# Optimization experiments

Hardware: AMD Instinct MI355X
Metric: run time of the kernel (lower is better)

## Reference

```python
import jax, jax.numpy as jnp
import numpy as np

# B groups, N packed tokens/group, D model dim, H heads, L layers, FF mlp hidden,
# M samples packed per group, C classes, PD patch_dim, NF/NT freq/time pos tables
B, N, D, H, L, FF, M, C, PD, NF, NT = 4, 1024, 768, 12, 12, 3072, 8, 527, 256, 8, 64


def _ln(x, g, b, eps=1e-6):
    m = jnp.mean(x, -1, keepdims=True)
    v = jnp.mean((x - m) ** 2, -1, keepdims=True)
    return (x - m) * jax.lax.rsqrt(v + eps) * g + b


def _attn(xq, xkv, Wq, bq, Wkv, bkv, Wo, bo, allowed):
    # allowed: [b, i, j] bool; faithful to source: NO 1/sqrt(d_head) scaling.
    b, i, _ = xq.shape
    j = xkv.shape[1]
    q = (xq @ Wq + bq).reshape(b, i, H, -1).transpose(0, 2, 1, 3)
    k, v = jnp.split(xkv @ Wkv + bkv, 2, axis=-1)
    k = k.reshape(b, j, H, -1).transpose(0, 2, 1, 3)
    v = v.reshape(b, j, H, -1).transpose(0, 2, 1, 3)
    dots = jnp.einsum('bhid,bhjd->bhij', q, k)
    neg = -jnp.finfo(dots.dtype).max
    dots = jnp.where(allowed[:, None, :, :], dots, neg)
    a = jax.nn.softmax(dots, axis=-1)
    out = jnp.einsum('bhij,bhjd->bhid', a, v).transpose(0, 2, 1, 3).reshape(b, i, -1)
    return out @ Wo + bo


def setup_inputs() -> dict:
    ks = iter(jax.random.split(jax.random.key(0), 48))
    rn = lambda shape, s=0.02: jax.random.normal(next(ks), shape, jnp.float32) * s
    return {
        'patches': jax.random.normal(next(ks), (B, N, PD), jnp.float32),
        'sample_ids': jnp.sort(jax.random.randint(next(ks), (B, N), 0, M), axis=-1).astype(jnp.int32),
        'key_pad': jnp.ones((B, N), bool),
        'freq_idx': jax.random.randint(next(ks), (B, N), 0, NF).astype(jnp.int32),
        'time_idx': jax.random.randint(next(ks), (B, N), 0, NT).astype(jnp.int32),
        'patch_W': rn((PD, D)), 'patch_b': jnp.zeros((D,)),
        'pos_f': rn((NF, D), 1.0), 'pos_t': rn((NT, D), 1.0),
        'ln1_g': jnp.ones((L, D)), 'ln1_b': jnp.zeros((L, D)),
        'Wq': rn((L, D, D)), 'bq': jnp.zeros((L, D)),
        'Wkv': rn((L, D, 2 * D)), 'bkv': jnp.zeros((L, 2 * D)),
        'Wo': rn((L, D, D)), 'bo': jnp.zeros((L, D)),
        'ln2_g': jnp.ones((L, D)), 'ln2_b': jnp.zeros((L, D)),
        'W1': rn((L, D, FF)), 'b1': jnp.zeros((L, FF)),
        'W2': rn((L, FF, D)), 'b2': jnp.zeros((L, D)),
        'norm_g': jnp.ones((D,)), 'norm_b': jnp.zeros((D,)),
        'pool_q': rn((D,), 1.0),
        'pool_Wq': rn((D, D)), 'pool_bq': jnp.zeros((D,)),
        'pool_Wkv': rn((D, 2 * D)), 'pool_bkv': jnp.zeros((2 * D,)),
        'pool_Wo': rn((D, D)), 'pool_bo': jnp.zeros((D,)),
        'mln_g': jnp.ones((D,)), 'mln_b': jnp.zeros((D,)),
        'head_W': rn((D, C)), 'head_b': jnp.zeros((C,)),
    }


def reference(patches, sample_ids, key_pad, freq_idx, time_idx, patch_W, patch_b, pos_f, pos_t,
              ln1_g, ln1_b, Wq, bq, Wkv, bkv, Wo, bo, ln2_g, ln2_b, W1, b1, W2, b2,
              norm_g, norm_b, pool_q, pool_Wq, pool_bq, pool_Wkv, pool_bkv, pool_Wo, pool_bo,
              mln_g, mln_b, head_W, head_b):
    # patch embed + factorized freq/time positional embedding
    x = patches @ patch_W + patch_b + pos_f[freq_idx] + pos_t[time_idx]  # [B, N, D]
    # block-diagonal attention within each packed sample + key-padding mask
    same = sample_ids[:, :, None] == sample_ids[:, None, :]
    allowed = same & key_pad[:, None, :]
    for l in range(L):
        h = _ln(x, ln1_g[l], ln1_b[l])
        x = x + _attn(h, h, Wq[l], bq[l], Wkv[l], bkv[l], Wo[l], bo[l], allowed)
        h = _ln(x, ln2_g[l], ln2_b[l])
        x = x + (jax.nn.gelu(h @ W1[l] + b1[l], approximate=False) @ W2[l] + b2[l])
    x = _ln(x, norm_g, norm_b)
    # attention pooling: one learned query per packed sample, attends only its own tokens
    queries = jnp.broadcast_to(pool_q, (B, M, D))
    pool_allowed = (sample_ids[:, None, :] == jnp.arange(M)[None, :, None]) & key_pad[:, None, :]
    pooled = _attn(queries, x, pool_Wq, pool_bq, pool_Wkv, pool_bkv, pool_Wo, pool_bo, pool_allowed)
    return _ln(pooled, mln_g, mln_b) @ head_W + head_b  # [B, M, C]
```

## Files before the change

kernel.cpp:

```cpp
#include <hip/hip_runtime.h>
#include <hip/hip_bf16.h>
#include <math.h>

#define BB   4
#define NN   1024
#define DD   768
#define HHH  12
#define LLL  12
#define FFD  3072
#define MMM  8
#define CCC  527
#define PDIM 256

typedef unsigned short u16;
typedef __attribute__((ext_vector_type(8))) short bf16x8;
typedef __attribute__((ext_vector_type(4))) float f32x4;

__device__ inline float b2f(u16 x) {
    union { float f; unsigned u; } c; c.u = ((unsigned)x) << 16; return c.f;
}
__device__ inline u16 f2b(float f) {
    __hip_bfloat16 h = __float2bfloat16(f);
    return *reinterpret_cast<u16*>(&h);
}

__device__ __forceinline__ float gelu_fast(float v) {
    const float x = v * 0.70710678118f;
    const float xa = fabsf(x);
    const float tt = 1.f / (1.f + 0.3275911f * xa);
    const float poly = tt * (0.254829592f + tt * (-0.284496736f + tt * (1.421413741f +
                       tt * (-1.453152027f + tt * 1.061405429f))));
    float er = 1.f - poly * __expf(-xa * xa);
    er = (x < 0.f) ? -er : er;
    return 0.5f * v * (1.f + er);
}

__device__ __forceinline__ void gl_lds16(const u16* g, const u16* l) {
    __builtin_amdgcn_global_load_lds(
        (const __attribute__((address_space(1))) unsigned int*)(unsigned long long)g,
        (__attribute__((address_space(3))) unsigned int*)(unsigned)(unsigned long long)l,
        16, 0, 0);
}

__global__ void k_pad_norm(const void* __restrict__ p, unsigned char* __restrict__ out, int n) {
    __shared__ int isInt;
    const int t = threadIdx.x;
    if (t == 0) isInt = 1;
    __syncthreads();
    const unsigned* up = (const unsigned*)p;
    for (int i = t; i < n / 4; i += 1024) {
        unsigned v = up[i];
        if (v > 1u) isInt = 0;
    }
    __syncthreads();
    const int* ip = (const int*)p;
    const unsigned char* cp = (const unsigned char*)p;
    const int mode = isInt;
    for (int i = t; i < n; i += 1024)
        out[i] = mode ? (unsigned char)(ip[i] != 0) : (unsigned char)(cp[i] != 0);
}

__global__ __launch_bounds__(256) void k_transpose_cvt(
    const float* __restrict__ src, u16* __restrict__ dst,
    int K, int N, long srcLS, long dstLS)
{
    __shared__ float t[64][33];
    const float* s = src + (size_t)blockIdx.z * srcLS;
    u16* d = dst + (size_t)blockIdx.z * dstLS;
    const int n0 = blockIdx.x * 32, k0 = blockIdx.y * 64;
    const int tx = threadIdx.x & 31, ty = threadIdx.x >> 5;
    #pragma unroll
    for (int i = 0; i < 8; i++)
        t[ty * 8 + i][tx] = s[(size_t)(k0 + ty * 8 + i) * N + n0 + tx];
    __syncthreads();
    #pragma unroll
    for (int p = 0; p < 4; p++) {
        const int ny = p * 8 + ty;
        union { u16 h[2]; unsigned u; } o;
        o.h[0] = f2b(t[2 * tx][ny]);
        o.h[1] = f2b(t[2 * tx + 1][ny]);
        *(unsigned*)&d[(size_t)(n0 + ny) * K + k0 + 2 * tx] = o.u;
    }
}

__global__ __launch_bounds__(256) void k_cvt(const float* __restrict__ s, u16* __restrict__ d, int n4) {
    int i = blockIdx.x * 256 + threadIdx.x;
    if (i >= n4) return;
    float4 v = ((const float4*)s)[i];
    union { u16 h[4]; uint2 u; } o;
    o.h[0] = f2b(v.x); o.h[1] = f2b(v.y); o.h[2] = f2b(v.z); o.h[3] = f2b(v.w);
    ((uint2*)d)[i] = o.u;
}

__global__ __launch_bounds__(256) void k_bias_pack(const float* __restrict__ bq,
                                                   const float* __restrict__ bkv,
                                                   float* __restrict__ bqkv) {
    int i = blockIdx.x * 256 + threadIdx.x;
    if (i >= LLL * 2304) return;
    int l = i / 2304, c = i % 2304;
    bqkv[i] = (c < 768) ? bq[l * 768 + c] : bkv[l * 1536 + (c - 768)];
}

__global__ void k_ranges(const int* __restrict__ sid, int2* __restrict__ qr, int2* __restrict__ pr) {
    int b = blockIdx.x, t = threadIdx.x;
    const int* s = sid + b * NN;
    if (t < 16) {
        int lo_id = s[t * 64], hi_id = s[t * 64 + 63];
        int lo = 0, hi = NN;
        while (lo < hi) { int mid = (lo + hi) >> 1; if (s[mid] < lo_id) lo = mid + 1; else hi = mid; }
        int l2 = 0, h2 = NN;
        while (l2 < h2) { int mid = (l2 + h2) >> 1; if (s[mid] <= hi_id) l2 = mid + 1; else h2 = mid; }
        qr[b * 16 + t] = make_int2(lo, l2);
    }
    if (t < MMM) {
        int l2 = 0, h2 = NN;
        while (l2 < h2) { int mid = (l2 + h2) >> 1; if (s[mid] < t) l2 = mid + 1; else h2 = mid; }
        int l3 = 0, h3 = NN;
        while (l3 < h3) { int mid = (l3 + h3) >> 1; if (s[mid] <= t) l3 = mid + 1; else h3 = mid; }
        pr[b * MMM + t] = make_int2(l2, l3);
    }
}

__device__ inline void stv(u16* p, float v) { *p = f2b(v); }
__device__ inline void stv(float* p, float v) { *p = v; }

template <typename OT>
__global__ __launch_bounds__(256) void k_ln(const float* __restrict__ x,
                                            const float* __restrict__ g,
                                            const float* __restrict__ b,
                                            OT* __restrict__ out) {
    int row = blockIdx.x;
    const float* xr = x + (size_t)row * DD;
    int t = threadIdx.x;
    float v[3], s1 = 0.f, s2 = 0.f;
    #pragma unroll
    for (int i = 0; i < 3; i++) { v[i] = xr[t + i * 256]; s1 += v[i]; s2 += v[i] * v[i]; }
    #pragma unroll
    for (int o = 32; o; o >>= 1) { s1 += __shfl_xor(s1, o); s2 += __shfl_xor(s2, o); }
    __shared__ float a1[4], a2[4];
    int w = t >> 6;
    if ((t & 63) == 0) { a1[w] = s1; a2[w] = s2; }
    __syncthreads();
    s1 = a1[0] + a1[1] + a1[2] + a1[3];
    s2 = a2[0] + a2[1] + a2[2] + a2[3];
    float mean = s1 * (1.f / DD);
    float var = s2 * (1.f / DD) - mean * mean;
    float rstd = rsqrtf(fmaxf(var, 0.f) + 1e-6f);
    #pragma unroll
    for (int i = 0; i < 3; i++) {
        int c = t + i * 256;
        stv(&out[(size_t)row * DD + c], (v[i] - mean) * rstd * g[c] + b[c]);
    }
}

template <int EPI, int BM>
__global__ __launch_bounds__(256) void k_gemm(
    const u16* __restrict__ A, int lda,
    const u16* __restrict__ Bt, int ldb,
    const float* __restrict__ bias,
    float* __restrict__ Cf, u16* __restrict__ Cb,
    const float* __restrict__ resid,
    int ldc, int K,
    const int* __restrict__ fidx = nullptr, const int* __restrict__ tidx = nullptr,
    const float* __restrict__ pf = nullptr, const float* __restrict__ pt = nullptr)
{
    constexpr int NR  = (BM == 128) ? 4 : 2;
    constexpr int ASZ = BM * 32;
    constexpr int BSZ = 128 * 32;
    __shared__ __align__(16) u16 As[3][ASZ];
    __shared__ __align__(16) u16 Bs[3][BSZ];
    const int gx = gridDim.x;
    const int nwg = gx * gridDim.y;
    int bid = blockIdx.y * gx + blockIdx.x;
    if ((nwg & 7) == 0) bid = (bid & 7) * (nwg >> 3) + (bid >> 3);
    const int row0 = (bid / gx) * BM, col0 = (bid % gx) * 128;
    const int t = threadIdx.x;
    const int w = t >> 6, lane = t & 63;
    const int wr = (BM == 128) ? (w >> 1) * 64 : 0;
    const int wc = (BM == 128) ? (w & 1) * 64 : w * 32;
    const int fr = lane & 15, fg = lane >> 4;
    const int srow = t >> 2, sseg = (t & 3) * 8;
    const u16* Ap = A + (size_t)(row0 + srow) * lda + sseg;
    const u16* Bp = Bt + (size_t)(col0 + srow) * ldb + sseg;
    const size_t lstep = (size_t)64 * lda, bstep = (size_t)64 * ldb;

    auto stage = [&](int buf, int k0) {
        #pragma unroll
        for (int i = 0; i < BM / 64; i++)
            gl_lds16(Ap + i * lstep + k0, &As[buf][i * 2048 + t * 8]);
        #pragma unroll
        for (int i = 0; i < 2; i++)
            gl_lds16(Bp + i * bstep + k0, &Bs[buf][i * 2048 + t * 8]);
    };

    f32x4 acc[4][NR];
    #pragma unroll
    for (int m = 0; m < 4; m++)
        #pragma unroll
        for (int n = 0; n < NR; n++) acc[m][n] = (f32x4){0.f, 0.f, 0.f, 0.f};

    const int nt = K >> 5;
    stage(0, 0);
    stage(1, 32);

    for (int kt = 0; kt < nt; ++kt) {
        if (kt + 1 < nt) {
            if constexpr (BM == 128) asm volatile("s_waitcnt vmcnt(4)" ::: "memory");
            else                     asm volatile("s_waitcnt vmcnt(3)" ::: "memory");
        } else {
            asm volatile("s_waitcnt vmcnt(0)" ::: "memory");
        }
        __builtin_amdgcn_s_barrier();
        __builtin_amdgcn_sched_barrier(0);
        if (kt + 2 < nt) stage((kt + 2) % 3, (kt + 2) * 32);
        const int cur = kt % 3;
        bf16x8 af[4], bfr[NR];
        #pragma unroll
        for (int m = 0; m < 4; m++) af[m] = *(const bf16x8*)&As[cur][(wr + m * 16 + fr) * 32 + fg * 8];
        #pragma unroll
        for (int n = 0; n < NR; n++) bfr[n] = *(const bf16x8*)&Bs[cur][(wc + n * 16 + fr) * 32 + fg * 8];
        __builtin_amdgcn_s_setprio(1);
        #pragma unroll
        for (int m = 0; m < 4; m++)
            #pragma unroll
            for (int n = 0; n < NR; n++)
                acc[m][n] = __builtin_amdgcn_mfma_f32_16x16x32_bf16(af[m], bfr[n], acc[m][n], 0, 0, 0);
        __builtin_amdgcn_s_setprio(0);
    }
    #pragma unroll
    for (int m = 0; m < 4; m++) {
        #pragma unroll
        for (int n = 0; n < NR; n++) {
            const int col = col0 + wc + n * 16 + fr;
            const float bb = bias[col];
            #pragma unroll
            for (int r = 0; r < 4; r++) {
                const size_t row = row0 + wr + m * 16 + fg * 4 + r;
                float v = acc[m][n][r] + bb;
                if (EPI == 0) {
                    Cb[row * ldc + col] = f2b(v);
                } else if (EPI == 1) {
                    Cf[row * ldc + col] = v + resid[row * ldc + col];
                } else if (EPI == 2) {
                    Cb[row * ldc + col] = f2b(gelu_fast(v));
                } else if (EPI == 3) {
                    Cf[row * ldc + col] = v;
                } else if (EPI == 5) {
                    const int fi = fidx[row], ti = tidx[row];
                    Cf[row * ldc + col] = v + pf[(size_t)fi * DD + col] + pt[(size_t)ti * DD + col];
                }
            }
        }
    }
}

__global__ __launch_bounds__(256) void k_attn(
    const u16* __restrict__ qkv,
    const int* __restrict__ sid, const unsigned char* __restrict__ pad,
    const int2* __restrict__ qr,
    u16* __restrict__ outb)
{
    __shared__ __align__(16) u16 Qs[64][72];
    __shared__ __align__(16) u16 Ks[64][72];
    __shared__ __align__(16) u16 VtL[64 * 72 + 32];
    __shared__ __align__(16) u16 Ps[4][16][72];
    __shared__ int sidq[64];
    __shared__ int sidj[64];
    __shared__ int padj[64];
    const int b = blockIdx.z, h = blockIdx.y, qt = blockIdx.x;
    const int i0 = qt * 64;
    const int t = threadIdx.x, w = t >> 6, lane = t & 63;
    const int fr = lane & 15, fg = lane >> 4;
    const int srow = t >> 2, sseg = (t & 3) * 16;
    const size_t tokbase = (size_t)b * NN;
    const u16* qbase = qkv + (tokbase + i0) * 2304 + h * 64;
    *(uint4*)&Qs[srow][sseg]     = *(const uint4*)(qbase + (size_t)srow * 2304 + sseg);
    *(uint4*)&Qs[srow][sseg + 8] = *(const uint4*)(qbase + (size_t)srow * 2304 + sseg + 8);
    if (t < 64) sidq[t] = sid[tokbase + i0 + t];
    __syncthreads();
    bf16x8 qf0 = *(const bf16x8*)&Qs[w * 16 + fr][fg * 8];
    bf16x8 qf1 = *(const bf16x8*)&Qs[w * 16 + fr][32 + fg * 8];
    const int myrow = w * 16 + fg * 4;
    float m_run[4], l_run[4];
    f32x4 oacc[4];
    #pragma unroll
    for (int r = 0; r < 4; r++) { m_run[r] = -1e30f; l_run[r] = 0.f; }
    #pragma unroll
    for (int n = 0; n < 4; n++) oacc[n] = (f32x4){0.f, 0.f, 0.f, 0.f};
    const int2 rg = qr[b * 16 + qt];
    const u16* kbase = qkv + tokbase * 2304 + 768 + h * 64;
    const u16* vbase = qkv + tokbase * 2304 + 1536 + h * 64;

    uint4 rk0, rk1, rv0, rv1;
    int rsid = 0, rpad = 0;
    const int jstart = rg.x & ~63;
    {
        const size_t ro = (size_t)(jstart + srow) * 2304;
        rk0 = *(const uint4*)(kbase + ro + sseg);
        rk1 = *(const uint4*)(kbase + ro + sseg + 8);
        rv0 = *(const uint4*)(vbase + ro + sseg);
        rv1 = *(const uint4*)(vbase + ro + sseg + 8);
        if (t < 64) { rsid = sid[tokbase + jstart + t]; rpad = pad[tokbase + jstart + t]; }
    }

    for (int j0 = jstart; j0 < rg.y; j0 += 64) {
        __syncthreads();
        *(uint4*)&Ks[srow][sseg]     = rk0;
        *(uint4*)&Ks[srow][sseg + 8] = rk1;
        {
            u16 tmp[16];
            *(uint4*)&tmp[0] = rv0;
            *(uint4*)&tmp[8] = rv1;
            const int goff = (sseg >> 4) << 3;
            #pragma unroll
            for (int e = 0; e < 16; e++)
                VtL[(sseg + e) * 72 + goff + srow] = tmp[e];
        }
        if (t < 64) { sidj[t] = rsid; padj[t] = rpad; }
        __syncthreads();
        if (j0 + 64 < rg.y) {
            const size_t ro = (size_t)(j0 + 64 + srow) * 2304;
            rk0 = *(const uint4*)(kbase + ro + sseg);
            rk1 = *(const uint4*)(kbase + ro + sseg + 8);
            rv0 = *(const uint4*)(vbase + ro + sseg);
            rv1 = *(const uint4*)(vbase + ro + sseg + 8);
            if (t < 64) { rsid = sid[tokbase + j0 + 64 + t]; rpad = pad[tokbase + j0 + 64 + t]; }
        }
        f32x4 s[4];
        __builtin_amdgcn_s_setprio(1);
        #pragma unroll
        for (int nj = 0; nj < 4; nj++) {
            bf16x8 kf0 = *(const bf16x8*)&Ks[nj * 16 + fr][fg * 8];
            bf16x8 kf1 = *(const bf16x8*)&Ks[nj * 16 + fr][32 + fg * 8];
            f32x4 a = (f32x4){0.f, 0.f, 0.f, 0.f};
            a = __builtin_amdgcn_mfma_f32_16x16x32_bf16(qf0, kf0, a, 0, 0, 0);
            a = __builtin_amdgcn_mfma_f32_16x16x32_bf16(qf1, kf1, a, 0, 0, 0);
            s[nj] = a;
        }
        __builtin_amdgcn_s_setprio(0);
        #pragma unroll
        for (int nj = 0; nj < 4; nj++) {
            const int jj = nj * 16 + fr;
            const int sj = sidj[jj];
            const int pd = padj[jj];
            #pragma unroll
            for (int r = 0; r < 4; r++) {
                const bool ok = pd && (sj == sidq[myrow + r]);
                s[nj][r] = ok ? s[nj][r] : -3e38f;
            }
        }
        float mnew[4], scale[4];
        #pragma unroll
        for (int r = 0; r < 4; r++) {
            float mx = fmaxf(fmaxf(s[0][r], s[1][r]), fmaxf(s[2][r], s[3][r]));
            #pragma unroll
            for (int o = 1; o < 16; o <<= 1) mx = fmaxf(mx, __shfl_xor(mx, o));
            mnew[r] = fmaxf(m_run[r], mx);
            scale[r] = __expf(m_run[r] - mnew[r]);
            m_run[r] = mnew[r];
        }
        #pragma unroll
        for (int r = 0; r < 4; r++) {
            float rs = 0.f;
            #pragma unroll
            for (int nj = 0; nj < 4; nj++) {
                float pv = __expf(s[nj][r] - mnew[r]);
                rs += pv;
                Ps[w][fg * 4 + r][nj * 16 + fr] = f2b(pv);
            }
            #pragma unroll
            for (int o = 1; o < 16; o <<= 1) rs += __shfl_xor(rs, o);
            l_run[r] = l_run[r] * scale[r] + rs;
        }
        #pragma unroll
        for (int n = 0; n < 4; n++)
            #pragma unroll
            for (int r = 0; r < 4; r++) oacc[n][r] *= scale[r];
        bf16x8 pa0 = *(const bf16x8*)&Ps[w][fr][fg * 8];
        bf16x8 pa1 = *(const bf16x8*)&Ps[w][fr][32 + fg * 8];
        __builtin_amdgcn_s_setprio(1);
        #pragma unroll
        for (int nd = 0; nd < 4; nd++) {
            bf16x8 vf0 = *(const bf16x8*)&VtL[(nd * 16 + fr) * 72 + nd * 8 + fg * 8];
            bf16x8 vf1 = *(const bf16x8*)&VtL[(nd * 16 + fr) * 72 + nd * 8 + 32 + fg * 8];
            oacc[nd] = __builtin_amdgcn_mfma_f32_16x16x32_bf16(pa0, vf0, oacc[nd], 0, 0, 0);
            oacc[nd] = __builtin_amdgcn_mfma_f32_16x16x32_bf16(pa1, vf1, oacc[nd], 0, 0, 0);
        }
        __builtin_amdgcn_s_setprio(0);
    }
    float inv[4];
    #pragma unroll
    for (int r = 0; r < 4; r++) inv[r] = 1.f / l_run[r];
    #pragma unroll
    for (int nd = 0; nd < 4; nd++)
        #pragma unroll
        for (int r = 0; r < 4; r++)
            outb[(tokbase + i0 + myrow + r) * DD + h * 64 + nd * 16 + fr] = f2b(oacc[nd][r] * inv[r]);
}

__global__ __launch_bounds__(64) void k_qvec(const float* __restrict__ pq, const float* __restrict__ Wq,
                                             const float* __restrict__ bq, float* __restrict__ qv) {
    int c = blockIdx.x;
    int l = threadIdx.x;
    float s = 0.f;
    #pragma unroll
    for (int d = l; d < DD; d += 64) s += pq[d] * Wq[(size_t)d * DD + c];
    #pragma unroll
    for (int o = 32; o; o >>= 1) s += __shfl_xor(s, o);
    if (l == 0) qv[c] = s + bq[c];
}

__global__ __launch_bounds__(256) void k_pool_attn(
    const float* __restrict__ qv, const u16* __restrict__ kv,
    const unsigned char* __restrict__ pad, const int2* __restrict__ pr,
    float* __restrict__ outp)
{
    const int idx = blockIdx.x;
    const int h = idx % HHH, bm = idx / HHH;
    const int b = bm >> 3, m = bm & 7;
    const int2 rg = pr[b * MMM + m];
    const int lo = rg.x, cnt = rg.y - rg.x;
    __shared__ float sc[NN];
    __shared__ float qsh[64];
    __shared__ float rbuf[4];
    __shared__ float vacc[4][64];
    if (threadIdx.x < 64) qsh[threadIdx.x] = qv[h * 64 + threadIdx.x];
    __syncthreads();
    for (int j = threadIdx.x; j < cnt; j += 256) {
        const u16* krow = kv + (size_t)(b * NN + lo + j) * 1536 + h * 64;
        float s = 0.f;
        #pragma unroll
        for (int dv = 0; dv < 8; dv++) {
            bf16x8 k8 = *(const bf16x8*)(krow + dv * 8);
            #pragma unroll
            for (int e = 0; e < 8; e++) s += qsh[dv * 8 + e] * b2f((u16)k8[e]);
        }
        sc[j] = pad[b * NN + lo + j] ? s : -3e38f;
    }
    __syncthreads();
    float mx = -3e38f;
    for (int j = threadIdx.x; j < cnt; j += 256) mx = fmaxf(mx, sc[j]);
    #pragma unroll
    for (int o = 32; o; o >>= 1) mx = fmaxf(mx, __shfl_xor(mx, o));
    if ((threadIdx.x & 63) == 0) rbuf[threadIdx.x >> 6] = mx;
    __syncthreads();
    mx = fmaxf(fmaxf(rbuf[0], rbuf[1]), fmaxf(rbuf[2], rbuf[3]));
    __syncthreads();
    float sm = 0.f;
    for (int j = threadIdx.x; j < cnt; j += 256) { float p = __expf(sc[j] - mx); sc[j] = p; sm += p; }
    #pragma unroll
    for (int o = 32; o; o >>= 1) sm += __shfl_xor(sm, o);
    if ((threadIdx.x & 63) == 0) rbuf[threadIdx.x >> 6] = sm;
    __syncthreads();
    sm = rbuf[0] + rbuf[1] + rbuf[2] + rbuf[3];
    const float inv = 1.f / sm;
    {
        const int d = threadIdx.x & 63, g = threadIdx.x >> 6;
        float acc = 0.f;
        for (int j = g; j < cnt; j += 4)
            acc += sc[j] * b2f(kv[(size_t)(b * NN + lo + j) * 1536 + 768 + h * 64 + d]);
        vacc[g][d] = acc;
        __syncthreads();
        if (g == 0)
            outp[(size_t)(b * MMM + m) * DD + h * 64 + d] =
                (vacc[0][d] + vacc[1][d] + vacc[2][d] + vacc[3][d]) * inv;
    }
}

__global__ __launch_bounds__(256) void k_small_mm(const float* __restrict__ A, const float* __restrict__ W,
                                                  const float* __restrict__ bias, float* __restrict__ out,
                                                  int N, int Kd) {
    const int row = blockIdx.y;
    const int cl = threadIdx.x & 63, kg = threadIdx.x >> 6;
    const int c = blockIdx.x * 64 + cl;
    const int cload = (c < N) ? c : (N - 1);
    __shared__ float As[DD];
    __shared__ float red[4][64];
    for (int d = threadIdx.x; d < Kd; d += 256) As[d] = A[(size_t)row * Kd + d];
    __syncthreads();
    const int kper = Kd >> 2;
    const int kbase = kg * kper;
    float s = 0.f;
    const float* w = W + (size_t)kbase * N + cload;
    #pragma unroll 4
    for (int i = 0; i < kper; i++) s += As[kbase + i] * w[(size_t)i * N];
    red[kg][cl] = s;
    __syncthreads();
    if (kg == 0 && c < N)
        out[(size_t)row * N + c] = red[0][cl] + red[1][cl] + red[2][cl] + red[3][cl] + bias[c];
}

extern "C" void kernel_launch(void* const* d_in, const int* in_sizes, int n_in,
                              void* d_out, int out_size, void* d_ws, size_t ws_size,
                              hipStream_t stream) {
    const float* patches   = (const float*)d_in[0];
    const int*   sample_ids= (const int*)d_in[1];
    const void*  key_pad_raw = (const void*)d_in[2];
    const int*   freq_idx  = (const int*)d_in[3];
    const int*   time_idx  = (const int*)d_in[4];
    const float* patch_W   = (const float*)d_in[5];
    const float* patch_b   = (const float*)d_in[6];
    const float* pos_f     = (const float*)d_in[7];
    const float* pos_t     = (const float*)d_in[8];
    const float* ln1_g     = (const float*)d_in[9];
    const float* ln1_b     = (const float*)d_in[10];
    const float* Wq        = (const float*)d_in[11];
    const float* bq        = (const float*)d_in[12];
    const float* Wkv       = (const float*)d_in[13];
    const float* bkv       = (const float*)d_in[14];
    const float* Wo        = (const float*)d_in[15];
    const float* bo        = (const float*)d_in[16];
    const float* ln2_g     = (const float*)d_in[17];
    const float* ln2_b     = (const float*)d_in[18];
    const float* W1        = (const float*)d_in[19];
    const float* b1        = (const float*)d_in[20];
    const float* W2        = (const float*)d_in[21];
    const float* b2        = (const float*)d_in[22];
    const float* norm_g    = (const float*)d_in[23];
    const float* norm_b    = (const float*)d_in[24];
    const float* pool_q    = (const float*)d_in[25];
    const float* pool_Wq   = (const float*)d_in[26];
    const float* pool_bq   = (const float*)d_in[27];
    const float* pool_Wkv  = (const float*)d_in[28];
    const float* pool_bkv  = (const float*)d_in[29];
    const float* pool_Wo   = (const float*)d_in[30];
    const float* pool_bo   = (const float*)d_in[31];
    const float* mln_g     = (const float*)d_in[32];
    const float* mln_b     = (const float*)d_in[33];
    const float* head_W    = (const float*)d_in[34];
    const float* head_b    = (const float*)d_in[35];
    float* outp = (float*)d_out;
    (void)in_sizes; (void)n_in; (void)out_size; (void)ws_size;

    char* ws = (char*)d_ws;
    size_t off = 0;
    auto alloc = [&](size_t bytes) -> void* {
        void* p = (void*)(ws + off);
        off += (bytes + 255) & ~(size_t)255;
        return p;
    };
    u16* WqkvT    = (u16*)alloc((size_t)LLL * 2304 * 768 * 2);
    u16* WoT      = (u16*)alloc((size_t)LLL * 768 * 768 * 2);
    u16* W1T      = (u16*)alloc((size_t)LLL * 3072 * 768 * 2);
    u16* W2T      = (u16*)alloc((size_t)LLL * 768 * 3072 * 2);
    u16* patchWT  = (u16*)alloc((size_t)768 * 256 * 2);
    u16* poolWkvT = (u16*)alloc((size_t)1536 * 768 * 2);
    float* bqkv   = (float*)alloc((size_t)LLL * 2304 * 4);
    unsigned char* pad_u8 = (unsigned char*)alloc(BB * NN);
    float* x      = (float*)alloc((size_t)4096 * 768 * 4);
    u16* hbuf     = (u16*)alloc((size_t)4096 * 768 * 2);
    u16* qkvb     = (u16*)alloc((size_t)4096 * 2304 * 2);
    u16* attno    = (u16*)alloc((size_t)4096 * 768 * 2);
    u16* mid      = (u16*)alloc((size_t)4096 * 3072 * 2);
    u16* patch_bf = mid;
    u16* xn       = attno;
    u16* poolkv   = qkvb;
    float* qvec   = (float*)alloc(768 * 4);
    float* pooled_pre = (float*)alloc(32 * 768 * 4);
    float* pooled2    = (float*)alloc(32 * 768 * 4);
    float* mlnout     = (float*)alloc(32 * 768 * 4);
    int2* qr = (int2*)alloc(4 * 16 * sizeof(int2));
    int2* pr = (int2*)alloc(4 * 8 * sizeof(int2));

    k_pad_norm<<<1, 1024, 0, stream>>>(key_pad_raw, pad_u8, BB * NN);
    k_transpose_cvt<<<dim3(24, 12, LLL), 256, 0, stream>>>(Wq, WqkvT, 768, 768, (long)768 * 768, (long)2304 * 768);
    k_transpose_cvt<<<dim3(48, 12, LLL), 256, 0, stream>>>(Wkv, WqkvT + (size_t)768 * 768, 768, 1536, (long)768 * 1536, (long)2304 * 768);
    k_transpose_cvt<<<dim3(24, 12, LLL), 256, 0, stream>>>(Wo, WoT, 768, 768, (long)768 * 768, (long)768 * 768);
    k_transpose_cvt<<<dim3(96, 12, LLL), 256, 0, stream>>>(W1, W1T, 768, 3072, (long)768 * 3072, (long)3072 * 768);
    k_transpose_cvt<<<dim3(24, 48, LLL), 256, 0, stream>>>(W2, W2T, 3072, 768, (long)3072 * 768, (long)768 * 3072);
    k_transpose_cvt<<<dim3(24, 4, 1), 256, 0, stream>>>(patch_W, patchWT, 256, 768, 0, 0);
    k_transpose_cvt<<<dim3(48, 12, 1), 256, 0, stream>>>(pool_Wkv, poolWkvT, 768, 1536, 0, 0);
    k_cvt<<<1024, 256, 0, stream>>>(patches, patch_bf, 4096 * 256 / 4);
    k_bias_pack<<<(LLL * 2304 + 255) / 256, 256, 0, stream>>>(bq, bkv, bqkv);
    k_ranges<<<4, 64, 0, stream>>>(sample_ids, qr, pr);

    k_gemm<5, 64><<<dim3(6, 64), 256, 0, stream>>>(patch_bf, 256, patchWT, 256, patch_b, x, nullptr, nullptr,
                                                   768, 256, freq_idx, time_idx, pos_f, pos_t);

    for (int l = 0; l < LLL; l++) {
        k_ln<u16><<<4096, 256, 0, stream>>>(x, ln1_g + l * 768, ln1_b + l * 768, hbuf);
        k_gemm<0, 128><<<dim3(18, 32), 256, 0, stream>>>(hbuf, 768, WqkvT + (size_t)l * 2304 * 768, 768,
                                                         bqkv + l * 2304, nullptr, qkvb, nullptr, 2304, 768);
        k_attn<<<dim3(16, 12, 4), 256, 0, stream>>>(qkvb, sample_ids, pad_u8, qr, attno);
        k_gemm<1, 64><<<dim3(6, 64), 256, 0, stream>>>(attno, 768, WoT + (size_t)l * 768 * 768, 768,
                                                       bo + l * 768, x, nullptr, x, 768, 768);
        k_ln<u16><<<4096, 256, 0, stream>>>(x, ln2_g + l * 768, ln2_b + l * 768, hbuf);
        k_gemm<2, 128><<<dim3(24, 32), 256, 0, stream>>>(hbuf, 768, W1T + (size_t)l * 3072 * 768, 768,
                                                         b1 + l * 3072, nullptr, mid, nullptr, 3072, 768);
        k_gemm<1, 64><<<dim3(6, 64), 256, 0, stream>>>(mid, 3072, W2T + (size_t)l * 768 * 3072, 3072,
                                                       b2 + l * 768, x, nullptr, x, 768, 3072);
    }

    k_ln<u16><<<4096, 256, 0, stream>>>(x, norm_g, norm_b, xn);
    k_gemm<0, 128><<<dim3(12, 32), 256, 0, stream>>>(xn, 768, poolWkvT, 768, pool_bkv, nullptr, poolkv, nullptr, 1536, 768);
    k_qvec<<<768, 64, 0, stream>>>(pool_q, pool_Wq, pool_bq, qvec);
    k_pool_attn<<<BB * MMM * HHH, 256, 0, stream>>>(qvec, poolkv, pad_u8, pr, pooled_pre);
    k_small_mm<<<dim3(12, 32), 256, 0, stream>>>(pooled_pre, pool_Wo, pool_bo, pooled2, 768, 768);
    k_ln<float><<<32, 256, 0, stream>>>(pooled2, mln_g, mln_b, mlnout);
    k_small_mm<<<dim3(9, 32), 256, 0, stream>>>(mlnout, head_W, head_b, outp, 527, 768);
}
```

Baseline: 2.063 ms.

## Double-buffer K/V tiles in attention and use one wave per row in layernorm

The attention kernel now keeps two shared-memory K/V buffers. The next tile is written while the current one is being computed, which cuts the two barriers per iteration down to one. Q staging and P share a single pooled LDS buffer. Layernorm now gives each row to one 64-lane wave with float4 loads and vector stores, which removes the cross-wave shared reduction and barrier. The trade-off is more LDS use per attention block, which could lower occupancy.

```diff
diff --git a/kernel.cpp b/kernel.cpp
--- a/kernel.cpp
+++ b/kernel.cpp
@@ -121,35 +121,44 @@
     }
 }
 
-__device__ inline void stv(u16* p, float v) { *p = f2b(v); }
-__device__ inline void stv(float* p, float v) { *p = v; }
-
 template <typename OT>
 __global__ __launch_bounds__(256) void k_ln(const float* __restrict__ x,
                                             const float* __restrict__ g,
                                             const float* __restrict__ b,
                                             OT* __restrict__ out) {
-    int row = blockIdx.x;
+    const int row = blockIdx.x * 4 + (threadIdx.x >> 6);
+    const int l = threadIdx.x & 63;
     const float* xr = x + (size_t)row * DD;
-    int t = threadIdx.x;
-    float v[3], s1 = 0.f, s2 = 0.f;
-    #pragma unroll
-    for (int i = 0; i < 3; i++) { v[i] = xr[t + i * 256]; s1 += v[i]; s2 += v[i] * v[i]; }
+    float4 v[3];
+    float s1 = 0.f, s2 = 0.f;
+    #pragma unroll
+    for (int k = 0; k < 3; k++) {
+        v[k] = *(const float4*)(xr + k * 256 + l * 4);
+        s1 += v[k].x + v[k].y + v[k].z + v[k].w;
+        s2 += v[k].x * v[k].x + v[k].y * v[k].y + v[k].z * v[k].z + v[k].w * v[k].w;
+    }
     #pragma unroll
     for (int o = 32; o; o >>= 1) { s1 += __shfl_xor(s1, o); s2 += __shfl_xor(s2, o); }
-    __shared__ float a1[4], a2[4];
-    int w = t >> 6;
-    if ((t & 63) == 0) { a1[w] = s1; a2[w] = s2; }
-    __syncthreads();
-    s1 = a1[0] + a1[1] + a1[2] + a1[3];
-    s2 = a2[0] + a2[1] + a2[2] + a2[3];
-    float mean = s1 * (1.f / DD);
-    float var = s2 * (1.f / DD) - mean * mean;
-    float rstd = rsqrtf(fmaxf(var, 0.f) + 1e-6f);
-    #pragma unroll
-    for (int i = 0; i < 3; i++) {
-        int c = t + i * 256;
-        stv(&out[(size_t)row * DD + c], (v[i] - mean) * rstd * g[c] + b[c]);
+    const float mean = s1 * (1.f / DD);
+    const float var = s2 * (1.f / DD) - mean * mean;
+    const float rstd = rsqrtf(fmaxf(var, 0.f) + 1e-6f);
+    #pragma unroll
+    for (int k = 0; k < 3; k++) {
+        const int c = k * 256 + l * 4;
+        const float4 gg = *(const float4*)(g + c);
+        const float4 bb = *(const float4*)(b + c);
+        const float r0 = (v[k].x - mean) * rstd * gg.x + bb.x;
+        const float r1 = (v[k].y - mean) * rstd * gg.y + bb.y;
+        const float r2 = (v[k].z - mean) * rstd * gg.z + bb.z;
+        const float r3 = (v[k].w - mean) * rstd * gg.w + bb.w;
+        if constexpr (sizeof(OT) == 2) {
+            union { u16 h[4]; uint2 u; } o;
+            o.h[0] = f2b(r0); o.h[1] = f2b(r1); o.h[2] = f2b(r2); o.h[3] = f2b(r3);
+            *(uint2*)&out[(size_t)row * DD + c] = o.u;
+        } else {
+            float4 o = make_float4(r0, r1, r2, r3);
+            *(float4*)&out[(size_t)row * DD + c] = o;
+        }
     }
 }
 
@@ -260,26 +269,29 @@
     const int2* __restrict__ qr,
     u16* __restrict__ outb)
 {
-    __shared__ __align__(16) u16 Qs[64][72];
-    __shared__ __align__(16) u16 Ks[64][72];
-    __shared__ __align__(16) u16 VtL[64 * 72 + 32];
-    __shared__ __align__(16) u16 Ps[4][16][72];
+    __shared__ __align__(16) u16 pool[2 * 4608 + 2 * 4640 + 4608];
+    u16* const K0  = pool;
+    u16* const K1  = pool + 4608;
+    u16* const V0  = pool + 9216;
+    u16* const V1  = pool + 9216 + 4640;
+    u16* const PsB = pool + 9216 + 9280;
     __shared__ int sidq[64];
-    __shared__ int sidj[64];
-    __shared__ int padj[64];
+    __shared__ int sidj[2][64];
+    __shared__ int padj[2][64];
     const int b = blockIdx.z, h = blockIdx.y, qt = blockIdx.x;
     const int i0 = qt * 64;
     const int t = threadIdx.x, w = t >> 6, lane = t & 63;
     const int fr = lane & 15, fg = lane >> 4;
     const int srow = t >> 2, sseg = (t & 3) * 16;
+    const int goff = (sseg >> 4) << 3;
     const size_t tokbase = (size_t)b * NN;
     const u16* qbase = qkv + (tokbase + i0) * 2304 + h * 64;
-    *(uint4*)&Qs[srow][sseg]     = *(const uint4*)(qbase + (size_t)srow * 2304 + sseg);
-    *(uint4*)&Qs[srow][sseg + 8] = *(const uint4*)(qbase + (size_t)srow * 2304 + sseg + 8);
+    *(uint4*)&K1[srow * 72 + sseg]     = *(const uint4*)(qbase + (size_t)srow * 2304 + sseg);
+    *(uint4*)&K1[srow * 72 + sseg + 8] = *(const uint4*)(qbase + (size_t)srow * 2304 + sseg + 8);
     if (t < 64) sidq[t] = sid[tokbase + i0 + t];
     __syncthreads();
-    bf16x8 qf0 = *(const bf16x8*)&Qs[w * 16 + fr][fg * 8];
-    bf16x8 qf1 = *(const bf16x8*)&Qs[w * 16 + fr][32 + fg * 8];
+    const bf16x8 qf0 = *(const bf16x8*)&K1[(w * 16 + fr) * 72 + fg * 8];
+    const bf16x8 qf1 = *(const bf16x8*)&K1[(w * 16 + fr) * 72 + 32 + fg * 8];
     const int myrow = w * 16 + fg * 4;
     float m_run[4], l_run[4];
     f32x4 oacc[4];
@@ -290,48 +302,50 @@
     const int2 rg = qr[b * 16 + qt];
     const u16* kbase = qkv + tokbase * 2304 + 768 + h * 64;
     const u16* vbase = qkv + tokbase * 2304 + 1536 + h * 64;
+    const int jstart = rg.x & ~63;
+    const int ntiles = (rg.y - jstart + 63) >> 6;
 
     uint4 rk0, rk1, rv0, rv1;
     int rsid = 0, rpad = 0;
-    const int jstart = rg.x & ~63;
-    {
-        const size_t ro = (size_t)(jstart + srow) * 2304;
+    auto load_tile = [&](int tile) {
+        const size_t ro = (size_t)(jstart + tile * 64 + srow) * 2304;
         rk0 = *(const uint4*)(kbase + ro + sseg);
         rk1 = *(const uint4*)(kbase + ro + sseg + 8);
         rv0 = *(const uint4*)(vbase + ro + sseg);
         rv1 = *(const uint4*)(vbase + ro + sseg + 8);
-        if (t < 64) { rsid = sid[tokbase + jstart + t]; rpad = pad[tokbase + jstart + t]; }
-    }
-
-    for (int j0 = jstart; j0 < rg.y; j0 += 64) {
-        __syncthreads();
-        *(uint4*)&Ks[srow][sseg]     = rk0;
-        *(uint4*)&Ks[srow][sseg + 8] = rk1;
-        {
-            u16 tmp[16];
-            *(uint4*)&tmp[0] = rv0;
-            *(uint4*)&tmp[8] = rv1;
-            const int goff = (sseg >> 4) << 3;
-            #pragma unroll
-            for (int e = 0; e < 16; e++)
-                VtL[(sseg + e) * 72 + goff + srow] = tmp[e];
-        }
-        if (t < 64) { sidj[t] = rsid; padj[t] = rpad; }
-        __syncthreads();
-        if (j0 + 64 < rg.y) {
-            const size_t ro = (size_t)(j0 + 64 + srow) * 2304;
-            rk0 = *(const uint4*)(kbase + ro + sseg);
-            rk1 = *(const uint4*)(kbase + ro + sseg + 8);
-            rv0 = *(const uint4*)(vbase + ro + sseg);
-            rv1 = *(const uint4*)(vbase + ro + sseg + 8);
-            if (t < 64) { rsid = sid[tokbase + j0 + 64 + t]; rpad = pad[tokbase + j0 + 64 + t]; }
+        if (t < 64) { rsid = sid[tokbase + jstart + tile * 64 + t]; rpad = pad[tokbase + jstart + tile * 64 + t]; }
+    };
+    auto write_tile = [&](u16* kb, u16* vb, int slot) {
+        *(uint4*)&kb[srow * 72 + sseg]     = rk0;
+        *(uint4*)&kb[srow * 72 + sseg + 8] = rk1;
+        u16 tmp[16];
+        *(uint4*)&tmp[0] = rv0;
+        *(uint4*)&tmp[8] = rv1;
+        #pragma unroll
+        for (int e = 0; e < 16; e++)
+            vb[(sseg + e) * 72 + goff + srow] = tmp[e];
+        if (t < 64) { sidj[slot][t] = rsid; padj[slot][t] = rpad; }
+    };
+
+    load_tile(0);
+    write_tile(K0, V0, 0);
+    if (ntiles > 1) load_tile(1);
+    __syncthreads();
+
+    for (int tt = 0; tt < ntiles; ++tt) {
+        const int cb = tt & 1;
+        u16* const kb = cb ? K1 : K0;
+        u16* const vb = cb ? V1 : V0;
+        if (tt + 1 < ntiles) {
+            write_tile(cb ? K0 : K1, cb ? V0 : V1, cb ^ 1);
+            if (tt + 2 < ntiles) load_tile(tt + 2);
         }
         f32x4 s[4];
         __builtin_amdgcn_s_setprio(1);
         #pragma unroll
         for (int nj = 0; nj < 4; nj++) {
-            bf16x8 kf0 = *(const bf16x8*)&Ks[nj * 16 + fr][fg * 8];
-            bf16x8 kf1 = *(const bf16x8*)&Ks[nj * 16 + fr][32 + fg * 8];
+            bf16x8 kf0 = *(const bf16x8*)&kb[(nj * 16 + fr) * 72 + fg * 8];
+            bf16x8 kf1 = *(const bf16x8*)&kb[(nj * 16 + fr) * 72 + 32 + fg * 8];
             f32x4 a = (f32x4){0.f, 0.f, 0.f, 0.f};
             a = __builtin_amdgcn_mfma_f32_16x16x32_bf16(qf0, kf0, a, 0, 0, 0);
             a = __builtin_amdgcn_mfma_f32_16x16x32_bf16(qf1, kf1, a, 0, 0, 0);
@@ -341,8 +355,8 @@
         #pragma unroll
         for (int nj = 0; nj < 4; nj++) {
             const int jj = nj * 16 + fr;
-            const int sj = sidj[jj];
-            const int pd = padj[jj];
+            const int sj = sidj[cb][jj];
+            const int pd = padj[cb][jj];
             #pragma unroll
             for (int r = 0; r < 4; r++) {
                 const bool ok = pd && (sj == sidq[myrow + r]);
@@ -366,7 +380,7 @@
             for (int nj = 0; nj < 4; nj++) {
                 float pv = __expf(s[nj][r] - mnew[r]);
                 rs += pv;
-                Ps[w][fg * 4 + r][nj * 16 + fr] = f2b(pv);
+                PsB[(w * 16 + fg * 4 + r) * 72 + nj * 16 + fr] = f2b(pv);
             }
             #pragma unroll
             for (int o = 1; o < 16; o <<= 1) rs += __shfl_xor(rs, o);
@@ -376,17 +390,18 @@
         for (int n = 0; n < 4; n++)
             #pragma unroll
             for (int r = 0; r < 4; r++) oacc[n][r] *= scale[r];
-        bf16x8 pa0 = *(const bf16x8*)&Ps[w][fr][fg * 8];
-        bf16x8 pa1 = *(const bf16x8*)&Ps[w][fr][32 + fg * 8];
+        bf16x8 pa0 = *(const bf16x8*)&PsB[(w * 16 + fr) * 72 + fg * 8];
+        bf16x8 pa1 = *(const bf16x8*)&PsB[(w * 16 + fr) * 72 + 32 + fg * 8];
         __builtin_amdgcn_s_setprio(1);
         #pragma unroll
         for (int nd = 0; nd < 4; nd++) {
-            bf16x8 vf0 = *(const bf16x8*)&VtL[(nd * 16 + fr) * 72 + nd * 8 + fg * 8];
-            bf16x8 vf1 = *(const bf16x8*)&VtL[(nd * 16 + fr) * 72 + nd * 8 + 32 + fg * 8];
+            bf16x8 vf0 = *(const bf16x8*)&vb[(nd * 16 + fr) * 72 + nd * 8 + fg * 8];
+            bf16x8 vf1 = *(const bf16x8*)&vb[(nd * 16 + fr) * 72 + nd * 8 + 32 + fg * 8];
             oacc[nd] = __builtin_amdgcn_mfma_f32_16x16x32_bf16(pa0, vf0, oacc[nd], 0, 0, 0);
             oacc[nd] = __builtin_amdgcn_mfma_f32_16x16x32_bf16(pa1, vf1, oacc[nd], 0, 0, 0);
         }
         __builtin_amdgcn_s_setprio(0);
+        __syncthreads();
     }
     float inv[4];
     #pragma unroll
@@ -578,24 +593,24 @@
                                                    768, 256, freq_idx, time_idx, pos_f, pos_t);
 
     for (int l = 0; l < LLL; l++) {
-        k_ln<u16><<<4096, 256, 0, stream>>>(x, ln1_g + l * 768, ln1_b + l * 768, hbuf);
+        k_ln<u16><<<1024, 256, 0, stream>>>(x, ln1_g + l * 768, ln1_b + l * 768, hbuf);
         k_gemm<0, 128><<<dim3(18, 32), 256, 0, stream>>>(hbuf, 768, WqkvT + (size_t)l * 2304 * 768, 768,
                                                          bqkv + l * 2304, nullptr, qkvb, nullptr, 2304, 768);
         k_attn<<<dim3(16, 12, 4), 256, 0, stream>>>(qkvb, sample_ids, pad_u8, qr, attno);
         k_gemm<1, 64><<<dim3(6, 64), 256, 0, stream>>>(attno, 768, WoT + (size_t)l * 768 * 768, 768,
                                                        bo + l * 768, x, nullptr, x, 768, 768);
-        k_ln<u16><<<4096, 256, 0, stream>>>(x, ln2_g + l * 768, ln2_b + l * 768, hbuf);
+        k_ln<u16><<<1024, 256, 0, stream>>>(x, ln2_g + l * 768, ln2_b + l * 768, hbuf);
         k_gemm<2, 128><<<dim3(24, 32), 256, 0, stream>>>(hbuf, 768, W1T + (size_t)l * 3072 * 768, 768,
                                                          b1 + l * 3072, nullptr, mid, nullptr, 3072, 768);
         k_gemm<1, 64><<<dim3(6, 64), 256, 0, stream>>>(mid, 3072, W2T + (size_t)l * 768 * 3072, 3072,
                                                        b2 + l * 768, x, nullptr, x, 768, 3072);
     }
 
-    k_ln<u16><<<4096, 256, 0, stream>>>(x, norm_g, norm_b, xn);
+    k_ln<u16><<<1024, 256, 0, stream>>>(x, norm_g, norm_b, xn);
     k_gemm<0, 128><<<dim3(12, 32), 256, 0, stream>>>(xn, 768, poolWkvT, 768, pool_bkv, nullptr, poolkv, nullptr, 1536, 768);
     k_qvec<<<768, 64, 0, stream>>>(pool_q, pool_Wq, pool_bq, qvec);
     k_pool_attn<<<BB * MMM * HHH, 256, 0, stream>>>(qvec, poolkv, pad_u8, pr, pooled_pre);
     k_small_mm<<<dim3(12, 32), 256, 0, stream>>>(pooled_pre, pool_Wo, pool_bo, pooled2, 768, 768);
-    k_ln<float><<<32, 256, 0, stream>>>(pooled2, mln_g, mln_b, mlnout);
+    k_ln<float><<<8, 256, 0, stream>>>(pooled2, mln_g, mln_b, mlnout);
     k_small_mm<<<dim3(9, 32), 256, 0, stream>>>(mlnout, head_W, head_b, outp, 527, 768);
 }
```

Result: no change. 2.062 ms (-0.1%).
